# Performance work log

Measured on AMD Instinct MI355X. Metric: run time of the kernel, lower is better.

The kernel has to match this reference:

```python
import jax, jax.numpy as jnp
import numpy as np

# dims: batch, points, patches(groups), patch size, hidden, heads, layers, ffn
B, N, G, K, D, H, L, F = 32, 8192, 256, 32, 384, 6, 12, 1536
MASK_RATIO = 0.75
LEN_KEEP = int(G * (1 - MASK_RATIO))  # 64 visible tokens
HD = D // H


def _layernorm(x, g, b, eps=1e-5):
    m = jnp.mean(x, -1, keepdims=True)
    v = jnp.mean(jnp.square(x - m), -1, keepdims=True)
    return (x - m) * jax.lax.rsqrt(v + eps) * g + b


def _normalize_points(x):
    # normalize(): center = mid of bbox, radius = max distance to center (iso/diag)
    bmin = x.min(-2, keepdims=True)
    bmax = x.max(-2, keepdims=True)
    center = 0.5 * (bmin + bmax)
    radius = jnp.linalg.norm(x - center, axis=-1, keepdims=True).max(-2, keepdims=True)
    return (x - center) / radius


def _fps(x, num_samples):
    # farthest point sampling; sequential by nature -> fori_loop over G (fixed, small)
    b, n, _ = x.shape
    idxs = jnp.zeros((b, num_samples), jnp.int32)

    def body(i, state):
        dists, idxs, last = state
        lastpt = jnp.take_along_axis(x, last[:, None, None].astype(jnp.int32), axis=1)  # [B,1,3]
        d = jnp.sum(jnp.square(x - lastpt), -1)  # [B,N]
        dists = jnp.minimum(dists, d)
        nxt = jnp.argmax(dists, -1).astype(jnp.int32)
        return dists, idxs.at[:, i].set(nxt), nxt

    dists0 = jnp.full((b, n), 1e10, x.dtype)
    _, idxs, _ = jax.lax.fori_loop(1, num_samples, body, (dists0, idxs, jnp.zeros((b,), jnp.int32)))
    return idxs


def _group(x, centers):
    # squared pairwise distances without materializing [B,G,N,3]
    d2 = (jnp.sum(jnp.square(centers), -1)[:, :, None]
          + jnp.sum(jnp.square(x), -1)[:, None, :]
          - 2.0 * jnp.einsum('bgc,bnc->bgn', centers, x))  # [B,G,N]
    _, idx = jax.lax.top_k(-d2, K)  # [B,G,K] knn indices
    nbrs = jnp.take_along_axis(x[:, None, :, :], idx[..., None], axis=2)  # [B,G,K,3] (_knn_gather)
    return nbrs - centers[:, :, None, :]


def setup_inputs() -> dict:
    key = jax.random.key(0)
    ks = iter(jax.random.split(key, 24))

    def w(shape, scale=0.02):
        return jax.random.normal(next(ks), shape, jnp.float32) * scale

    ones_ln = jnp.stack([jnp.ones(D, jnp.float32), jnp.zeros(D, jnp.float32)])
    return {
        'points': jax.random.normal(next(ks), (B, N, 3), jnp.float32),
        'noise': jax.random.uniform(next(ks), (B, G), jnp.float32),
        # mini-PointNet patch encoder
        'pe_w1': w((3, 128)), 'pe_b1': jnp.zeros((128,), jnp.float32),
        'pe_w2': w((128, 256)), 'pe_b2': jnp.zeros((256,), jnp.float32),
        'pe_w3': w((256, D)), 'pe_b3': jnp.zeros((D,), jnp.float32),
        # positional MLP on patch centers
        'pos_w1': w((3, 128)), 'pos_b1': jnp.zeros((128,), jnp.float32),
        'pos_w2': w((128, D)), 'pos_b2': jnp.zeros((D,), jnp.float32),
        # transformer (stacked over L layers)
        'ln1': jnp.tile(ones_ln[None], (L, 1, 1)),
        'wqkv': w((L, D, 3 * D)), 'bqkv': jnp.zeros((L, 3 * D), jnp.float32),
        'wo': w((L, D, D)), 'bo': jnp.zeros((L, D), jnp.float32),
        'ln2': jnp.tile(ones_ln[None], (L, 1, 1)),
        'wi': w((L, D, F)), 'bi': jnp.zeros((L, F), jnp.float32),
        'wo2': w((L, F, D)), 'bo2': jnp.zeros((L, D), jnp.float32),
        'lnf': ones_ln,
    }


def _forward(points, noise, pe_w1, pe_b1, pe_w2, pe_b2, pe_w3, pe_b3,
             pos_w1, pos_b1, pos_w2, pos_b2,
             ln1, wqkv, bqkv, wo, bo, ln2, wi, bi, wo2, bo2, lnf):
    x = _normalize_points(points)
    cidx = _fps(x, G)                                        # [B,G]
    centers = jnp.take_along_axis(x, cidx[..., None], axis=1)  # [B,G,3]
    patches = _group(x, centers)                              # [B,G,K,3]

    # patch encode (per-point MLP -> max pool -> proj)
    f = jax.nn.relu(patches @ pe_w1 + pe_b1)
    f = f @ pe_w2 + pe_b2
    tokens = f.max(axis=2) @ pe_w3 + pe_b3                    # [B,G,D]
    pos = jax.nn.relu(centers @ pos_w1 + pos_b1) @ pos_w2 + pos_b2  # [B,G,D]

    # mask(): argsort-of-noise shuffle, keep first len_keep tokens
    ids_shuffle = jnp.argsort(noise, axis=1)
    ids_keep = ids_shuffle[:, :LEN_KEEP]                      # [B,64]
    h = (jnp.take_along_axis(tokens, ids_keep[..., None], axis=1)
         + jnp.take_along_axis(pos, ids_keep[..., None], axis=1))  # [B,64,D]

    scale = 1.0 / jnp.sqrt(jnp.asarray(HD, h.dtype))

    def layer(h, p):
        l1, wq, bq, wo_, bo_, l2, wi_, bi_, wo2_, bo2_ = p
        y = _layernorm(h, l1[0], l1[1])
        qkv = (y @ wq + bq).reshape(B, LEN_KEEP, 3, H, HD)  # '(three h d)' split
        q, k, v = jnp.moveaxis(qkv, 2, 0)
        a = jax.nn.softmax(jnp.einsum('bshd,bthd->bhst', q, k) * scale, -1)
        o = jnp.einsum('bhst,bthd->bshd', a, v).reshape(B, LEN_KEEP, D)
        h = h + o @ wo_ + bo_
        y = _layernorm(h, l2[0], l2[1])
        h = h + jax.nn.gelu(y @ wi_ + bi_) @ wo2_ + bo2_
        return h, None

    h, _ = jax.lax.scan(layer, h, (ln1, wqkv, bqkv, wo, bo, ln2, wi, bi, wo2, bo2))
    return _layernorm(h, lnf[0], lnf[1])


def reference(points, noise, pe_w1, pe_b1, pe_w2, pe_b2, pe_w3, pe_b3,
              pos_w1, pos_b1, pos_w2, pos_b2,
              ln1, wqkv, bqkv, wo, bo, ln2, wi, bi, wo2, bo2, lnf):
    return _forward(points, noise, pe_w1, pe_b1, pe_w2, pe_b2, pe_w3, pe_b3,
                    pos_w1, pos_b1, pos_w2, pos_b2,
                    ln1, wqkv, bqkv, wo, bo, ln2, wi, bi, wo2, bo2, lnf)
```

## Files before the change

kernel.cpp:

```cpp
#include <hip/hip_runtime.h>

#define NPTS 8192
#define NB   32
#define NG   256
#define NK   32
#define ND   384
#define NH   6
#define NLK  64
#define NF   1536
#define NHD  64
#define NL   12
#define MM   2048

typedef unsigned short u16;
typedef unsigned long long u64;
typedef __attribute__((ext_vector_type(8))) short short8;
typedef __attribute__((ext_vector_type(16))) float f32x16;
typedef __attribute__((ext_vector_type(4))) unsigned short ushort4v;

#define PL_PRE   147456ull
#define PL_LAYER 1769472ull
#define WT_ELEMS (PL_PRE + 12ull*PL_LAYER)

__device__ __forceinline__ float bf2f(u16 v){
  unsigned int u = ((unsigned int)v) << 16;
  float f; __builtin_memcpy(&f, &u, 4); return f;
}
__device__ __forceinline__ float ldf(const void* p, size_t i, bool bf){
  if(bf) return bf2f(((const u16*)p)[i]);
  return ((const float*)p)[i];
}
__device__ __forceinline__ u16 f2bf(float f){
  unsigned int x; __builtin_memcpy(&x, &f, 4);
  x += 0x7fffu + ((x >> 16) & 1u);
  return (u16)(x >> 16);
}
__device__ __forceinline__ void split2(float v, u16& hi, u16& lo){
  hi = f2bf(v);
  lo = f2bf(v - bf2f(hi));
}

__global__ __launch_bounds__(256) void k_detect(const u16* __restrict__ pts,
                                                int* __restrict__ flag){
  __shared__ int bad;
  if(threadIdx.x==0) bad=0;
  __syncthreads();
  int hit=0;
  for(int i=threadIdx.x; i<4096; i+=256){
    unsigned e = (pts[i] >> 7) & 0xFFu;
    if(e >= 0x90u) hit=1;
  }
  if(hit) atomicOr(&bad, 1);
  __syncthreads();
  if(threadIdx.x==0) *flag = bad ? 0 : 1;
}

__device__ __forceinline__ float blockMax256(float v, float* sb, int tid){
  for(int off=32; off; off>>=1) v = fmaxf(v, __shfl_down(v, off));
  __syncthreads();
  if((tid&63)==0) sb[tid>>6] = v;
  __syncthreads();
  return fmaxf(fmaxf(sb[0],sb[1]), fmaxf(sb[2],sb[3]));
}

__global__ __launch_bounds__(256) void k_normalize(const void* __restrict__ pts,
                                                   float* __restrict__ xn,
                                                   const int* __restrict__ flag){
#pragma clang fp contract(off)
  int b = blockIdx.x, tid = threadIdx.x;
  const bool bf = flag[0] != 0;
  __shared__ float sb[4];
  const size_t base = (size_t)b*NPTS*3;
  float mn0=1e30f,mn1=1e30f,mn2=1e30f, mx0=-1e30f,mx1=-1e30f,mx2=-1e30f;
  for(int n=tid; n<NPTS; n+=256){
    float x0=ldf(pts,base+n*3,bf), x1=ldf(pts,base+n*3+1,bf), x2=ldf(pts,base+n*3+2,bf);
    mn0=fminf(mn0,x0); mx0=fmaxf(mx0,x0);
    mn1=fminf(mn1,x1); mx1=fmaxf(mx1,x1);
    mn2=fminf(mn2,x2); mx2=fmaxf(mx2,x2);
  }
  mx0=blockMax256(mx0,sb,tid); mn0=-blockMax256(-mn0,sb,tid);
  mx1=blockMax256(mx1,sb,tid); mn1=-blockMax256(-mn1,sb,tid);
  mx2=blockMax256(mx2,sb,tid); mn2=-blockMax256(-mn2,sb,tid);
  float c0=0.5f*(mn0+mx0), c1=0.5f*(mn1+mx1), c2=0.5f*(mn2+mx2);
  float mr=0.0f;
  for(int n=tid; n<NPTS; n+=256){
    float d0=ldf(pts,base+n*3,bf)-c0, d1=ldf(pts,base+n*3+1,bf)-c1, d2=ldf(pts,base+n*3+2,bf)-c2;
    float nr = sqrtf((d0*d0 + d1*d1) + d2*d2);
    mr = fmaxf(mr, nr);
  }
  float radius = blockMax256(mr, sb, tid);
  float* XO = xn + base;
  for(int n=tid; n<NPTS; n+=256){
    XO[n*3  ] = (ldf(pts,base+n*3  ,bf)-c0)/radius;
    XO[n*3+1] = (ldf(pts,base+n*3+1,bf)-c1)/radius;
    XO[n*3+2] = (ldf(pts,base+n*3+2,bf)-c2)/radius;
  }
}

__global__ __launch_bounds__(256) void k_keep(const void* __restrict__ noise,
                                              int* __restrict__ keep,
                                              const int* __restrict__ flag){
  int b = blockIdx.x, g = threadIdx.x;
  const bool bf = flag[0] != 0;
  __shared__ float nv[NG];
  nv[g] = ldf(noise, (size_t)b*NG+g, bf);
  __syncthreads();
  float v = nv[g]; int r = 0;
  for(int j=0; j<NG; j++){
    float u = nv[j];
    r += (u < v) || (u == v && j < g);
  }
  if(r < NLK) keep[b*NLK + r] = g;
}

__device__ __forceinline__ void kmax_dpp_step(unsigned& hi, unsigned& lo, unsigned oh, unsigned ol){
  bool g = (oh > hi) || (oh == hi && ol > lo);
  hi = g ? oh : hi; lo = g ? ol : lo;
}
#define KMAX_DPP(CTRL) { \
  unsigned oh=(unsigned)__builtin_amdgcn_update_dpp(0,(int)kh,(CTRL),0xf,0xf,true); \
  unsigned ol=(unsigned)__builtin_amdgcn_update_dpp(0,(int)kl,(CTRL),0xf,0xf,true); \
  kmax_dpp_step(kh,kl,oh,ol); }

__global__ __launch_bounds__(512) void k_fps_trans(
    const float* __restrict__ xn, float* __restrict__ centers,
    const void* __restrict__ pe_w3, const void* __restrict__ pos_w2,
    const void* __restrict__ wqkv, const void* __restrict__ wo,
    const void* __restrict__ wi,   const void* __restrict__ wo2,
    u16* __restrict__ wthi, u16* __restrict__ wtlo,
    const int* __restrict__ flag)
{
  __shared__ float xs[NPTS*3];
  __shared__ u64 skey[3];
  __shared__ int sc[NG];
  int tid = threadIdx.x;

  if(blockIdx.x >= 32){
    const bool bf = flag[0]!=0;
    float (*t)[33] = reinterpret_cast<float(*)[33]>(xs);
    int gid = blockIdx.x - 32;
    const void* W; int Kd, Nd; size_t woff, doff; int local;
    if(gid < 96){        W=pe_w3;  Kd=256; Nd=384; woff=0; doff=0;      local=gid; }
    else if(gid < 144){  W=pos_w2; Kd=128; Nd=384; woff=0; doff=98304;  local=gid-96; }
    else{
      int g2 = gid - 144; int l = g2 / 1728; int id = g2 % 1728;
      size_t lb = PL_PRE + (size_t)l*PL_LAYER;
      if(id < 432){        W=wqkv; Kd=384;  Nd=1152; woff=(size_t)l*442368; doff=lb;          local=id; }
      else if(id < 576){   W=wo;   Kd=384;  Nd=384;  woff=(size_t)l*147456; doff=lb+442368;   local=id-432; }
      else if(id < 1152){  W=wi;   Kd=384;  Nd=1536; woff=(size_t)l*589824; doff=lb+589824;   local=id-576; }
      else {               W=wo2;  Kd=1536; Nd=384;  woff=(size_t)l*589824; doff=lb+1179648;  local=id-1152; }
    }
    int ntiles = Nd >> 5;
    int n0 = (local % ntiles)*32, k0 = (local / ntiles)*32;
    for(int i=0;i<2;i++){
      int idx = tid + i*512; int kr = idx>>5, nc = idx&31;
      t[kr][nc] = ldf(W, woff + (size_t)(k0+kr)*Nd + n0+nc, bf);
    }
    __syncthreads();
    for(int i=0;i<2;i++){
      int idx = tid + i*512; int nr = idx>>5, kc = idx&31;
      float v = t[kc][nr];
      u16 hi,lo; split2(v,hi,lo);
      size_t o = doff + (size_t)(n0+nr)*Kd + k0+kc;
      wthi[o]=hi; wtlo[o]=lo;
    }
    return;
  }

  {
#pragma clang fp contract(off)
    int b = blockIdx.x;
    int lane = tid & 63;
    const float* X = xn + (size_t)b*NPTS*3;
    float px[16],py[16],pz[16],dd[16];
#pragma unroll
    for(int s=0;s<16;s++){
      int n = s*512 + tid;
      px[s]=X[n*3]; py[s]=X[n*3+1]; pz[s]=X[n*3+2];
      dd[s]=1e10f;
    }
    for(int i=tid; i<NPTS*3; i+=512) xs[i] = X[i];
    if(tid==0){ skey[0]=0ull; skey[1]=0ull; skey[2]=0ull; sc[0]=0; }
    __syncthreads();
    float lx = xs[0], ly = xs[1], lz = xs[2];
    for(int i=1;i<NG;i++){
      int c = i % 3;
      float bv=-1.0f; int bs=0;
#pragma unroll
      for(int s=0;s<16;s++){
        float dx=px[s]-lx, dy=py[s]-ly, dz=pz[s]-lz;
        float d=(dx*dx + dy*dy) + dz*dz;
        d = fminf(dd[s], d); dd[s]=d;
        if(d > bv){ bv=d; bs=s; }
      }
      int bn = bs*512 + tid;
      unsigned kh; __builtin_memcpy(&kh,&bv,4);
      unsigned kl = (unsigned)(NPTS-1-bn);
      KMAX_DPP(0x111)
      KMAX_DPP(0x112)
      KMAX_DPP(0x114)
      KMAX_DPP(0x118)
      KMAX_DPP(0x142)
      KMAX_DPP(0x143)
      if(lane==63) atomicMax(&skey[c], ((u64)kh<<32) | (u64)kl);
      __syncthreads();
      u64 k64 = skey[c];
      int n = (NPTS-1) - (int)(k64 & 0xFFFFFFFFull);
      n &= (NPTS-1);
      if(tid==0){ sc[i]=n; skey[(i+2)%3]=0ull; }
      lx = xs[n*3]; ly = xs[n*3+1]; lz = xs[n*3+2];
    }
    __syncthreads();
    if(tid < NG){
      int n = sc[tid] & (NPTS-1);
      centers[((size_t)b*NG+tid)*3  ] = xs[n*3];
      centers[((size_t)b*NG+tid)*3+1] = xs[n*3+1];
      centers[((size_t)b*NG+tid)*3+2] = xs[n*3+2];
    }
  }
}

__global__ __launch_bounds__(256) void k_knn(
    const float* __restrict__ xn, const float* __restrict__ centers,
    const int* __restrict__ keep, float* __restrict__ patches)
{
  int blk=blockIdx.x; int b=blk>>6; int j=blk&63; int tid=threadIdx.x;
  __shared__ float sd[NPTS];
  __shared__ int   sel[NK];
  __shared__ float rv[4]; __shared__ int rn[4];
  __shared__ int   sseln;
  int g = keep[b*NLK + j] & (NG-1);
  const float* C = centers + ((size_t)b*NG + g)*3;
  float c0=C[0], c1=C[1], c2=C[2];
  const float* X = xn + (size_t)b*NPTS*3;
  {
#pragma clang fp contract(off)
    float cc = (c0*c0 + c1*c1) + c2*c2;
    for(int n=tid; n<NPTS; n+=256){
      float x0=X[n*3], x1=X[n*3+1], x2=X[n*3+2];
      float xx=(x0*x0 + x1*x1) + x2*x2;
      float dt=(c0*x0 + c1*x1) + c2*x2;
      sd[n] = (cc + xx) - 2.0f*dt;
    }
  }
  __syncthreads();
  float dl[32];
  for(int s=0;s<32;s++) dl[s] = sd[s*256 + tid];
  unsigned int alive = 0xffffffffu;
  for(int r=0; r<NK; r++){
    float bv=1e30f; int bn=0x7fffffff;
    for(int s=0;s<32;s++){
      if(alive & (1u<<s)){
        float v = dl[s];
        if(v < bv){ bv=v; bn=s*256+tid; }
      }
    }
    for(int off=32;off;off>>=1){
      float ov=__shfl_down(bv,off); int on=__shfl_down(bn,off);
      if(ov<bv || (ov==bv && on<bn)){ bv=ov; bn=on; }
    }
    if((tid&63)==0){ rv[tid>>6]=bv; rn[tid>>6]=bn; }
    __syncthreads();
    if(tid==0){
      float v=rv[0]; int n=rn[0];
      for(int w=1;w<4;w++) if(rv[w]<v || (rv[w]==v && rn[w]<n)){ v=rv[w]; n=rn[w]; }
      n &= (NPTS-1);
      sseln=n; sel[r]=n;
    }
    __syncthreads();
    int n = sseln;
    if((n & 255) == tid) alive &= ~(1u << (n >> 8));
  }
  __syncthreads();
  if(tid < NK){
    int n = sel[tid] & (NPTS-1);
    float* P = patches + ((size_t)(b*NLK+j)*NK + tid)*3;
    P[0]=X[n*3  ]-c0;
    P[1]=X[n*3+1]-c1;
    P[2]=X[n*3+2]-c2;
  }
}

__global__ __launch_bounds__(256) void k_embed(
    const float* __restrict__ patches, const float* __restrict__ centers,
    const int* __restrict__ keep,
    const void* __restrict__ w1, const void* __restrict__ b1,
    const void* __restrict__ w2, const void* __restrict__ b2,
    const void* __restrict__ pw1, const void* __restrict__ pb1,
    u16* __restrict__ mfhi, u16* __restrict__ mflo,
    u16* __restrict__ phhi, u16* __restrict__ phlo,
    const int* __restrict__ flag)
{
  int blk=blockIdx.x; int b=blk>>6; int j=blk&63; int tid=threadIdx.x;
  const bool bf = flag[0] != 0;
  __shared__ float pat[NK*3];
  __shared__ __align__(16) float f1t[128*36];
  int row = b*NLK + j;
  if(tid < NK*3) pat[tid] = patches[(size_t)row*NK*3 + tid];
  __syncthreads();
  for(int i=0;i<16;i++){
    int idx = tid + i*256;
    int k = idx>>7, m = idx&127;
    float v = ldf(b1,m,bf)
            + pat[k*3+0]*ldf(w1,        m,bf)
            + pat[k*3+1]*ldf(w1, 128 + m,bf)
            + pat[k*3+2]*ldf(w1, 256 + m,bf);
    f1t[m*36 + k] = fmaxf(v, 0.0f);
  }
  __syncthreads();
  float acc[NK];
  {
    float bv = ldf(b2, tid, bf);
#pragma unroll
    for(int k=0;k<NK;k++) acc[k]=bv;
  }
  for(int jj=0;jj<128;jj++){
    float wv = ldf(w2, (size_t)jj*256+tid, bf);
    const float* fr = &f1t[jj*36];
#pragma unroll
    for(int k8=0;k8<8;k8++){
      float4 fv = *reinterpret_cast<const float4*>(fr + k8*4);
      acc[k8*4+0] = fmaf(fv.x, wv, acc[k8*4+0]);
      acc[k8*4+1] = fmaf(fv.y, wv, acc[k8*4+1]);
      acc[k8*4+2] = fmaf(fv.z, wv, acc[k8*4+2]);
      acc[k8*4+3] = fmaf(fv.w, wv, acc[k8*4+3]);
    }
  }
  float mx = acc[0];
#pragma unroll
  for(int k=1;k<NK;k++) mx = fmaxf(mx, acc[k]);
  { u16 hi,lo; split2(mx,hi,lo);
    mfhi[(size_t)row*256 + tid]=hi; mflo[(size_t)row*256 + tid]=lo; }
  if(tid < 128){
    int g = keep[b*NLK + j] & (NG-1);
    const float* C = centers + ((size_t)b*NG + g)*3;
    float v = ldf(pb1,tid,bf)
            + C[0]*ldf(pw1,        tid,bf)
            + C[1]*ldf(pw1, 128 + tid,bf)
            + C[2]*ldf(pw1, 256 + tid,bf);
    v = fmaxf(v, 0.0f);
    u16 hi,lo; split2(v,hi,lo);
    phhi[(size_t)row*128 + tid]=hi; phlo[(size_t)row*128 + tid]=lo;
  }
}

__global__ __launch_bounds__(256) void k_transpose4(
    const void* __restrict__ wqkv, const void* __restrict__ wo,
    const void* __restrict__ wi,   const void* __restrict__ wo2,
    int l, u16* __restrict__ dhi, u16* __restrict__ dlo,
    const int* __restrict__ flag){
  __shared__ float t[32][33];
  const bool bf = flag[0]!=0;
  int id = blockIdx.x;
  const void* W; int Kd, Nd; size_t woff, doff; int local;
  if(id < 432){        W=wqkv; Kd=384;  Nd=1152; woff=(size_t)l*442368; doff=PL_PRE;          local=id; }
  else if(id < 576){   W=wo;   Kd=384;  Nd=384;  woff=(size_t)l*147456; doff=PL_PRE+442368;   local=id-432; }
  else if(id < 1152){  W=wi;   Kd=384;  Nd=1536; woff=(size_t)l*589824; doff=PL_PRE+589824;   local=id-576; }
  else {               W=wo2;  Kd=1536; Nd=384;  woff=(size_t)l*589824; doff=PL_PRE+1179648;  local=id-1152; }
  int ntiles = Nd >> 5;
  int n0 = (local % ntiles)*32, k0 = (local / ntiles)*32;
  for(int i=0;i<4;i++){
    int idx = threadIdx.x + i*256; int kr = idx>>5, nc = idx&31;
    t[kr][nc] = ldf(W, woff + (size_t)(k0+kr)*Nd + n0+nc, bf);
  }
  __syncthreads();
  for(int i=0;i<4;i++){
    int idx = threadIdx.x + i*256; int nr = idx>>5, kc = idx&31;
    float v = t[kc][nr];
    u16 hi,lo; split2(v,hi,lo);
    size_t o = doff + (size_t)(n0+nr)*Kd + k0+kc;
    dhi[o]=hi; dlo[o]=lo;
  }
}

__global__ __launch_bounds__(128) void k_ln_split(const float* __restrict__ X,
                                                  const void* __restrict__ gb, size_t go,
                                                  u16* __restrict__ Yhi, u16* __restrict__ Ylo,
                                                  const int* __restrict__ flag){
  int row=blockIdx.x, tid=threadIdx.x;
  const bool bf = flag[0] != 0;
  const float* x = X + (size_t)row*ND;
  __shared__ float sbuf[2];
  float v0=x[tid], v1=x[tid+128], v2=x[tid+256];
  float s = v0+v1+v2;
  for(int off=32;off;off>>=1) s += __shfl_down(s,off);
  if((tid&63)==0) sbuf[tid>>6]=s;
  __syncthreads();
  float mean = (sbuf[0]+sbuf[1]) * (1.0f/(float)ND);
  __syncthreads();
  float d0=v0-mean, d1=v1-mean, d2=v2-mean;
  s = d0*d0 + d1*d1 + d2*d2;
  for(int off=32;off;off>>=1) s += __shfl_down(s,off);
  if((tid&63)==0) sbuf[tid>>6]=s;
  __syncthreads();
  float var = (sbuf[0]+sbuf[1]) * (1.0f/(float)ND);
  float rstd = 1.0f / sqrtf(var + 1e-5f);
  float o0 = d0*rstd*ldf(gb,go+tid    ,bf) + ldf(gb,go+ND+tid    ,bf);
  float o1 = d1*rstd*ldf(gb,go+tid+128,bf) + ldf(gb,go+ND+tid+128,bf);
  float o2 = d2*rstd*ldf(gb,go+tid+256,bf) + ldf(gb,go+ND+tid+256,bf);
  u16 hi,lo; size_t rb = (size_t)row*ND;
  split2(o0,hi,lo); Yhi[rb+tid    ]=hi; Ylo[rb+tid    ]=lo;
  split2(o1,hi,lo); Yhi[rb+tid+128]=hi; Ylo[rb+tid+128]=lo;
  split2(o2,hi,lo); Yhi[rb+tid+256]=hi; Ylo[rb+tid+256]=lo;
}

template<int TM, int TN, int ACT, bool RES, bool OSPLIT>
__global__ __launch_bounds__(256) void k_gemm_mfma(
    const u16* __restrict__ Ahi, const u16* __restrict__ Alo,
    const u16* __restrict__ Whi, const u16* __restrict__ Wlo, size_t wo,
    const void* __restrict__ bias, size_t bo, const int* __restrict__ flag,
    const float* __restrict__ res, float* __restrict__ Cf,
    u16* __restrict__ Ohi, u16* __restrict__ Olo,
    int N, int K)
{
  __shared__ __align__(16) u16 sAh[2][64*40];
  __shared__ __align__(16) u16 sAl[2][64*40];
  __shared__ __align__(16) u16 sBh[2][64*40];
  __shared__ __align__(16) u16 sBl[2][64*40];
  int tid = threadIdx.x;
  int wave = tid >> 6, lane = tid & 63;
  int wm = wave >> 1, wn = wave & 1;
  int l31 = lane & 31, half = lane >> 5;
  int row0 = blockIdx.y*TM, col0 = blockIdx.x*TN;
  const bool bf = flag[0] != 0;
  f32x16 acc;
#pragma unroll
  for(int r=0;r<16;r++) acc[r]=0.f;

  const int sr  = tid >> 2;
  const int scc = (tid & 3) * 8;
  const u16* gAh = Ahi + (size_t)(row0+sr)*K + scc;
  const u16* gAl = Alo + (size_t)(row0+sr)*K + scc;
  const u16* gBh = Whi + wo + (size_t)(col0+sr)*K + scc;
  const u16* gBl = Wlo + wo + (size_t)(col0+sr)*K + scc;
  const int ldst = sr*40 + scc;

  uint4 rah = *reinterpret_cast<const uint4*>(gAh);
  uint4 ral = *reinterpret_cast<const uint4*>(gAl);
  uint4 rbh = *reinterpret_cast<const uint4*>(gBh);
  uint4 rbl = *reinterpret_cast<const uint4*>(gBl);

  const int nk = K >> 5;
  for(int t=0; t<nk; ++t){
    const int buf = t & 1;
    *reinterpret_cast<uint4*>(&sAh[buf][ldst]) = rah;
    *reinterpret_cast<uint4*>(&sAl[buf][ldst]) = ral;
    *reinterpret_cast<uint4*>(&sBh[buf][ldst]) = rbh;
    *reinterpret_cast<uint4*>(&sBl[buf][ldst]) = rbl;
    __syncthreads();
    if(t+1 < nk){
      const int ko = (t+1) << 5;
      rah = *reinterpret_cast<const uint4*>(gAh + ko);
      ral = *reinterpret_cast<const uint4*>(gAl + ko);
      rbh = *reinterpret_cast<const uint4*>(gBh + ko);
      rbl = *reinterpret_cast<const uint4*>(gBl + ko);
    }
#pragma unroll
    for(int ks=0; ks<2; ks++){
      int aoff = (wm*32 + l31)*40 + ks*16 + half*8;
      int boff = (wn*32 + l31)*40 + ks*16 + half*8;
      short8 ah = *reinterpret_cast<const short8*>(&sAh[buf][aoff]);
      short8 al = *reinterpret_cast<const short8*>(&sAl[buf][aoff]);
      short8 bh = *reinterpret_cast<const short8*>(&sBh[buf][boff]);
      short8 bl = *reinterpret_cast<const short8*>(&sBl[buf][boff]);
      acc = __builtin_amdgcn_mfma_f32_32x32x16_bf16(ah, bh, acc, 0,0,0);
      acc = __builtin_amdgcn_mfma_f32_32x32x16_bf16(ah, bl, acc, 0,0,0);
      acc = __builtin_amdgcn_mfma_f32_32x32x16_bf16(al, bh, acc, 0,0,0);
    }
  }
  int col = col0 + wn*32 + l31;
  float bv = ldf(bias, bo+col, bf);
#pragma unroll
  for(int r=0;r<16;r++){
    int row = row0 + wm*32 + (r&3) + 8*(r>>2) + 4*half;
    float v = acc[r] + bv;
    if(ACT==1){
      float xx = v;
      v = 0.5f*xx*(1.0f + tanhf(0.7978845608028654f*(xx + 0.044715f*xx*xx*xx)));
    }
    if(RES) v += res[(size_t)row*N + col];
    if(OSPLIT){
      u16 hi,lo; split2(v,hi,lo);
      Ohi[(size_t)row*N + col]=hi; Olo[(size_t)row*N + col]=lo;
    }else{
      Cf[(size_t)row*N + col]=v;
    }
  }
}

__global__ __launch_bounds__(256) void k_attn_pl(const float* __restrict__ qkv,
                                                 u16* __restrict__ ohi,
                                                 u16* __restrict__ olo){
  __shared__ float Qt[64*68];
  __shared__ float Kt[64*68];
  __shared__ float V [64*68];
  __shared__ float SB[64*68];
  int blk=blockIdx.x; int b=blk/NH, h=blk%NH;
  int tid=threadIdx.x;
  for(int idx=tid; idx<4096; idx+=256){
    int s=idx>>6, d=idx&63;
    const float* r = qkv + ((size_t)(b*NLK+s))*1152 + h*NHD + d;
    Qt[d*68+s]=r[0];
    Kt[d*68+s]=r[384];
    V [s*68+d]=r[768];
  }
  __syncthreads();
  {
    const int i0 = (tid>>4)*4, j0 = (tid&15)*4;
    float a00=0.f,a01=0.f,a02=0.f,a03=0.f;
    float a10=0.f,a11=0.f,a12=0.f,a13=0.f;
    float a20=0.f,a21=0.f,a22=0.f,a23=0.f;
    float a30=0.f,a31=0.f,a32=0.f,a33=0.f;
#pragma unroll 4
    for(int d=0;d<64;d++){
      float4 qa = *reinterpret_cast<const float4*>(&Qt[d*68+i0]);
      float4 kb = *reinterpret_cast<const float4*>(&Kt[d*68+j0]);
      a00=fmaf(qa.x,kb.x,a00); a01=fmaf(qa.x,kb.y,a01); a02=fmaf(qa.x,kb.z,a02); a03=fmaf(qa.x,kb.w,a03);
      a10=fmaf(qa.y,kb.x,a10); a11=fmaf(qa.y,kb.y,a11); a12=fmaf(qa.y,kb.z,a12); a13=fmaf(qa.y,kb.w,a13);
      a20=fmaf(qa.z,kb.x,a20); a21=fmaf(qa.z,kb.y,a21); a22=fmaf(qa.z,kb.z,a22); a23=fmaf(qa.z,kb.w,a23);
      a30=fmaf(qa.w,kb.x,a30); a31=fmaf(qa.w,kb.y,a31); a32=fmaf(qa.w,kb.z,a32); a33=fmaf(qa.w,kb.w,a33);
    }
    float4 o0 = {a00*0.125f, a01*0.125f, a02*0.125f, a03*0.125f};
    float4 o1 = {a10*0.125f, a11*0.125f, a12*0.125f, a13*0.125f};
    float4 o2 = {a20*0.125f, a21*0.125f, a22*0.125f, a23*0.125f};
    float4 o3 = {a30*0.125f, a31*0.125f, a32*0.125f, a33*0.125f};
    *reinterpret_cast<float4*>(&SB[(i0  )*68+j0]) = o0;
    *reinterpret_cast<float4*>(&SB[(i0+1)*68+j0]) = o1;
    *reinterpret_cast<float4*>(&SB[(i0+2)*68+j0]) = o2;
    *reinterpret_cast<float4*>(&SB[(i0+3)*68+j0]) = o3;
  }
  __syncthreads();
  if(tid<64){
    float* rowp=&SB[tid*68];
    float m=rowp[0];
    for(int j=1;j<64;j++) m=fmaxf(m,rowp[j]);
    float sum=0.0f;
    for(int j=0;j<64;j++){ float e=__expf(rowp[j]-m); rowp[j]=e; sum+=e; }
    for(int j=0;j<64;j++) Qt[j*68+tid] = rowp[j]/sum;
  }
  __syncthreads();
  {
    const int s0 = (tid>>4)*4, d0 = (tid&15)*4;
    float a00=0.f,a01=0.f,a02=0.f,a03=0.f;
    float a10=0.f,a11=0.f,a12=0.f,a13=0.f;
    float a20=0.f,a21=0.f,a22=0.f,a23=0.f;
    float a30=0.f,a31=0.f,a32=0.f,a33=0.f;
#pragma unroll 4
    for(int t=0;t<64;t++){
      float4 av = *reinterpret_cast<const float4*>(&Qt[t*68+s0]);
      float4 vv = *reinterpret_cast<const float4*>(&V [t*68+d0]);
      a00=fmaf(av.x,vv.x,a00); a01=fmaf(av.x,vv.y,a01); a02=fmaf(av.x,vv.z,a02); a03=fmaf(av.x,vv.w,a03);
      a10=fmaf(av.y,vv.x,a10); a11=fmaf(av.y,vv.y,a11); a12=fmaf(av.y,vv.z,a12); a13=fmaf(av.y,vv.w,a13);
      a20=fmaf(av.z,vv.x,a20); a21=fmaf(av.z,vv.y,a21); a22=fmaf(av.z,vv.z,a22); a23=fmaf(av.z,vv.w,a23);
      a30=fmaf(av.w,vv.x,a30); a31=fmaf(av.w,vv.y,a31); a32=fmaf(av.w,vv.z,a32); a33=fmaf(av.w,vv.w,a33);
    }
    float rr[4][4] = {{a00,a01,a02,a03},{a10,a11,a12,a13},{a20,a21,a22,a23},{a30,a31,a32,a33}};
#pragma unroll
    for(int si=0; si<4; si++){
      ushort4v h4, l4;
#pragma unroll
      for(int di=0; di<4; di++){
        u16 hi,lo; split2(rr[si][di],hi,lo);
        h4[di]=hi; l4[di]=lo;
      }
      size_t o = ((size_t)(b*NLK+s0+si))*ND + h*NHD + d0;
      *reinterpret_cast<ushort4v*>(&ohi[o]) = h4;
      *reinterpret_cast<ushort4v*>(&olo[o]) = l4;
    }
  }
}

template<bool FINAL>
__global__ __launch_bounds__(128) void k_ln(const float* __restrict__ X,
                                            const void* __restrict__ gb, size_t go,
                                            void* __restrict__ Y,
                                            const int* __restrict__ flag){
  int row=blockIdx.x, tid=threadIdx.x;
  const bool bf = flag[0] != 0;
  const float* x = X + (size_t)row*ND;
  __shared__ float sbuf[2];
  float v0=x[tid], v1=x[tid+128], v2=x[tid+256];
  float s = v0+v1+v2;
  for(int off=32;off;off>>=1) s += __shfl_down(s,off);
  if((tid&63)==0) sbuf[tid>>6]=s;
  __syncthreads();
  float mean = (sbuf[0]+sbuf[1]) * (1.0f/(float)ND);
  __syncthreads();
  float d0=v0-mean, d1=v1-mean, d2=v2-mean;
  s = d0*d0 + d1*d1 + d2*d2;
  for(int off=32;off;off>>=1) s += __shfl_down(s,off);
  if((tid&63)==0) sbuf[tid>>6]=s;
  __syncthreads();
  float var = (sbuf[0]+sbuf[1]) * (1.0f/(float)ND);
  float rstd = 1.0f / sqrtf(var + 1e-5f);
  float o0 = d0*rstd*ldf(gb,go+tid    ,bf) + ldf(gb,go+ND+tid    ,bf);
  float o1 = d1*rstd*ldf(gb,go+tid+128,bf) + ldf(gb,go+ND+tid+128,bf);
  float o2 = d2*rstd*ldf(gb,go+tid+256,bf) + ldf(gb,go+ND+tid+256,bf);
  if(FINAL && bf){
    u16* yo = (u16*)Y + (size_t)row*ND;
    yo[tid]=f2bf(o0); yo[tid+128]=f2bf(o1); yo[tid+256]=f2bf(o2);
  }else{
    float* yo = (float*)Y + (size_t)row*ND;
    yo[tid]=o0; yo[tid+128]=o1; yo[tid+256]=o2;
  }
}

extern "C" void kernel_launch(void* const* d_in, const int* in_sizes, int n_in,
                              void* d_out, int out_size, void* d_ws, size_t ws_size,
                              hipStream_t stream){
  (void)in_sizes; (void)n_in; (void)out_size;
  const void* pts   = d_in[0];
  const void* noise = d_in[1];
  const void* pe_w1 = d_in[2];
  const void* pe_b1 = d_in[3];
  const void* pe_w2 = d_in[4];
  const void* pe_b2 = d_in[5];
  const void* pe_w3 = d_in[6];
  const void* pe_b3 = d_in[7];
  const void* pos_w1= d_in[8];
  const void* pos_b1= d_in[9];
  const void* pos_w2= d_in[10];
  const void* pos_b2= d_in[11];
  const void* ln1   = d_in[12];
  const void* wqkv  = d_in[13];
  const void* bqkv  = d_in[14];
  const void* wo    = d_in[15];
  const void* bo    = d_in[16];
  const void* ln2   = d_in[17];
  const void* wi    = d_in[18];
  const void* bi    = d_in[19];
  const void* wo2   = d_in[20];
  const void* bo2   = d_in[21];
  const void* lnf   = d_in[22];

  const size_t needed_small = (6711296ull + 16) * 4;
  if (ws_size < needed_small) return;
  const size_t wt_f32_off = 6711312ull;
  const size_t needed_big = (wt_f32_off + WT_ELEMS) * 4;
  const bool big = ws_size >= needed_big;

  float* ws   = (float*)d_ws;
  float* h    = ws;
  u16*  yhi   = (u16*)(ws + 786432);
  u16*  ylo   = yhi + 786432;
  float* qkvb = ws + 1572864;
  u16*  athi  = (u16*)(ws + 3932160);
  u16*  atlo  = athi + 786432;
  u16*  ubhi  = (u16*)(ws + 1572864);
  u16*  ublo  = ubhi + 3145728;
  float* xn   = ws + 1572864;
  float* patches;
  float* centers;
  int*   keep;
  int*   flag;
  u16 *wthi, *wtlo;
  if(big){
    patches = ws + 6488064;
    centers = ws + 6684672;
    keep    = (int*)(ws + 6709248);
    flag    = (int*)(ws + 6711296);
    wthi    = (u16*)(ws + wt_f32_off);
    wtlo    = wthi + WT_ELEMS;
  }else{
    wthi    = (u16*)(ws + 4718592);
    wtlo    = (u16*)(ws + 5677056);
    patches = ws + 6635520;
    centers = ws + 6832128;
    keep    = (int*)(ws + 6856704);
    flag    = (int*)(ws + 6858752);
    if(ws_size < (6858752ull + 16) * 4) return;
  }

  k_detect   <<<1, 256, 0, stream>>>((const u16*)pts, flag);
  k_normalize<<<NB, 256, 0, stream>>>(pts, xn, flag);
  k_keep     <<<NB, 256, 0, stream>>>(noise, keep, flag);
  {
    int grid = big ? (32 + 144 + 12*1728) : (32 + 144);
    k_fps_trans<<<grid, 512, 0, stream>>>(xn, centers, pe_w3, pos_w2,
        wqkv, wo, wi, wo2, wthi, wtlo, flag);
  }
  k_knn      <<<NB*NLK, 256, 0, stream>>>(xn, centers, keep, patches);
  k_embed    <<<NB*NLK, 256, 0, stream>>>(patches, centers, keep,
      pe_w1, pe_b1, pe_w2, pe_b2, pos_w1, pos_b1,
      yhi , yhi + 2048*256 , athi , athi + 2048*128 , flag);
  k_gemm_mfma<64,64,0,false,false><<<dim3(6,32), 256, 0, stream>>>(
      yhi, yhi + 2048*256, wthi, wtlo, 0, pe_b3, 0, flag, nullptr, h, nullptr, nullptr, 384, 256);
  k_gemm_mfma<64,64,0,true ,false><<<dim3(6,32), 256, 0, stream>>>(
      athi, athi + 2048*128, wthi, wtlo, 98304, pos_b2, 0, flag, h, h, nullptr, nullptr, 384, 128);

  for(int l=0; l<NL; l++){
    size_t lb = big ? (PL_PRE + (size_t)l*PL_LAYER) : PL_PRE;
    if(!big){
      k_transpose4<<<1728, 256, 0, stream>>>(wqkv, wo, wi, wo2, l, wthi, wtlo, flag);
    }
    k_ln_split<<<MM, 128, 0, stream>>>(h, ln1, (size_t)l*2*ND, yhi, ylo, flag);
    k_gemm_mfma<64,64,0,false,false><<<dim3(18,32), 256, 0, stream>>>(
        yhi, ylo, wthi, wtlo, lb, bqkv, (size_t)l*1152, flag, nullptr, qkvb, nullptr, nullptr, 1152, 384);
    k_attn_pl<<<NB*NH, 256, 0, stream>>>(qkvb, athi, atlo);
    k_gemm_mfma<64,64,0,true ,false><<<dim3(6,32), 256, 0, stream>>>(
        athi, atlo, wthi, wtlo, lb + 442368, bo, (size_t)l*384, flag, h, h, nullptr, nullptr, 384, 384);
    k_ln_split<<<MM, 128, 0, stream>>>(h, ln2, (size_t)l*2*ND, yhi, ylo, flag);
    k_gemm_mfma<64,64,1,false,true ><<<dim3(24,32), 256, 0, stream>>>(
        yhi, ylo, wthi, wtlo, lb + 589824, bi, (size_t)l*1536, flag, nullptr, nullptr, ubhi, ublo, 1536, 384);
    k_gemm_mfma<64,64,0,true ,false><<<dim3(6,32), 256, 0, stream>>>(
        ubhi, ublo, wthi, wtlo, lb + 1179648, bo2, (size_t)l*384, flag, h, h, nullptr, nullptr, 384, 1536);
  }
  k_ln<true><<<MM, 128, 0, stream>>>(h, lnf, 0, d_out, flag);
}
```

Before: 1.815 ms.

## Shrink GEMM row tile to 32, fold keep into FPS kernel, fast GELU tanh

The MFMA GEMMs now use a 32-row tile with 128 threads. Each thread loads two B rows so the 64-column tile is still filled, and the grid doubles to give more blocks for the small M=2048 matrices. The separate k_keep launch is merged into the FPS/transpose kernel as 32 extra blocks, which removes one launch. The tanh in the GELU epilogue is replaced by an exp-based formula. This trades less A-tile reuse per block and slightly different tanh rounding for better occupancy and lower launch overhead.

```diff
diff --git a/kernel.cpp b/kernel.cpp
--- a/kernel.cpp
+++ b/kernel.cpp
@@ -97,22 +97,6 @@
   }
 }
 
-__global__ __launch_bounds__(256) void k_keep(const void* __restrict__ noise,
-                                              int* __restrict__ keep,
-                                              const int* __restrict__ flag){
-  int b = blockIdx.x, g = threadIdx.x;
-  const bool bf = flag[0] != 0;
-  __shared__ float nv[NG];
-  nv[g] = ldf(noise, (size_t)b*NG+g, bf);
-  __syncthreads();
-  float v = nv[g]; int r = 0;
-  for(int j=0; j<NG; j++){
-    float u = nv[j];
-    r += (u < v) || (u == v && j < g);
-  }
-  if(r < NLK) keep[b*NLK + r] = g;
-}
-
 __device__ __forceinline__ void kmax_dpp_step(unsigned& hi, unsigned& lo, unsigned oh, unsigned ol){
   bool g = (oh > hi) || (oh == hi && ol > lo);
   hi = g ? oh : hi; lo = g ? ol : lo;
@@ -124,6 +108,7 @@
 
 __global__ __launch_bounds__(512) void k_fps_trans(
     const float* __restrict__ xn, float* __restrict__ centers,
+    const void* __restrict__ noise, int* __restrict__ keep,
     const void* __restrict__ pe_w3, const void* __restrict__ pos_w2,
     const void* __restrict__ wqkv, const void* __restrict__ wo,
     const void* __restrict__ wi,   const void* __restrict__ wo2,
@@ -135,10 +120,10 @@
   __shared__ int sc[NG];
   int tid = threadIdx.x;
 
-  if(blockIdx.x >= 32){
+  if(blockIdx.x >= 64){
     const bool bf = flag[0]!=0;
     float (*t)[33] = reinterpret_cast<float(*)[33]>(xs);
-    int gid = blockIdx.x - 32;
+    int gid = blockIdx.x - 64;
     const void* W; int Kd, Nd; size_t woff, doff; int local;
     if(gid < 96){        W=pe_w3;  Kd=256; Nd=384; woff=0; doff=0;      local=gid; }
     else if(gid < 144){  W=pos_w2; Kd=128; Nd=384; woff=0; doff=98304;  local=gid-96; }
@@ -163,6 +148,23 @@
       u16 hi,lo; split2(v,hi,lo);
       size_t o = doff + (size_t)(n0+nr)*Kd + k0+kc;
       wthi[o]=hi; wtlo[o]=lo;
+    }
+    return;
+  }
+
+  if(blockIdx.x >= 32){
+    const bool bf = flag[0]!=0;
+    int b = blockIdx.x - 32;
+    float* nv = xs;
+    if(tid < NG) nv[tid] = ldf(noise, (size_t)b*NG+tid, bf);
+    __syncthreads();
+    if(tid < NG){
+      float v = nv[tid]; int r = 0;
+      for(int j=0; j<NG; j++){
+        float u = nv[j];
+        r += (u < v) || (u == v && j < tid);
+      }
+      if(r < NLK) keep[b*NLK + r] = tid;
     }
     return;
   }
@@ -404,8 +406,8 @@
   split2(o2,hi,lo); Yhi[rb+tid+256]=hi; Ylo[rb+tid+256]=lo;
 }
 
-template<int TM, int TN, int ACT, bool RES, bool OSPLIT>
-__global__ __launch_bounds__(256) void k_gemm_mfma(
+template<int TM, int ACT, bool RES, bool OSPLIT>
+__global__ __launch_bounds__((TM==32)?128:256) void k_gemm_mfma(
     const u16* __restrict__ Ahi, const u16* __restrict__ Alo,
     const u16* __restrict__ Whi, const u16* __restrict__ Wlo, size_t wo,
     const void* __restrict__ bias, size_t bo, const int* __restrict__ flag,
@@ -413,10 +415,11 @@
     u16* __restrict__ Ohi, u16* __restrict__ Olo,
     int N, int K)
 {
-  __shared__ __align__(16) u16 sAh[2][64*40];
-  __shared__ __align__(16) u16 sAl[2][64*40];
-  __shared__ __align__(16) u16 sBh[2][64*40];
-  __shared__ __align__(16) u16 sBl[2][64*40];
+  constexpr int TN = 64;
+  __shared__ __align__(16) u16 sAh[2][TM*40];
+  __shared__ __align__(16) u16 sAl[2][TM*40];
+  __shared__ __align__(16) u16 sBh[2][TN*40];
+  __shared__ __align__(16) u16 sBl[2][TN*40];
   int tid = threadIdx.x;
   int wave = tid >> 6, lane = tid & 63;
   int wm = wave >> 1, wn = wave & 1;
@@ -439,6 +442,11 @@
   uint4 ral = *reinterpret_cast<const uint4*>(gAl);
   uint4 rbh = *reinterpret_cast<const uint4*>(gBh);
   uint4 rbl = *reinterpret_cast<const uint4*>(gBl);
+  uint4 rbh1, rbl1;
+  if constexpr (TM==32){
+    rbh1 = *reinterpret_cast<const uint4*>(gBh + 32*(size_t)K);
+    rbl1 = *reinterpret_cast<const uint4*>(gBl + 32*(size_t)K);
+  }
 
   const int nk = K >> 5;
   for(int t=0; t<nk; ++t){
@@ -447,6 +455,10 @@
     *reinterpret_cast<uint4*>(&sAl[buf][ldst]) = ral;
     *reinterpret_cast<uint4*>(&sBh[buf][ldst]) = rbh;
     *reinterpret_cast<uint4*>(&sBl[buf][ldst]) = rbl;
+    if constexpr (TM==32){
+      *reinterpret_cast<uint4*>(&sBh[buf][ldst + 32*40]) = rbh1;
+      *reinterpret_cast<uint4*>(&sBl[buf][ldst + 32*40]) = rbl1;
+    }
     __syncthreads();
     if(t+1 < nk){
       const int ko = (t+1) << 5;
@@ -454,6 +466,10 @@
       ral = *reinterpret_cast<const uint4*>(gAl + ko);
       rbh = *reinterpret_cast<const uint4*>(gBh + ko);
       rbl = *reinterpret_cast<const uint4*>(gBl + ko);
+      if constexpr (TM==32){
+        rbh1 = *reinterpret_cast<const uint4*>(gBh + 32*(size_t)K + ko);
+        rbl1 = *reinterpret_cast<const uint4*>(gBl + 32*(size_t)K + ko);
+      }
     }
 #pragma unroll
     for(int ks=0; ks<2; ks++){
@@ -476,7 +492,12 @@
     float v = acc[r] + bv;
     if(ACT==1){
       float xx = v;
-      v = 0.5f*xx*(1.0f + tanhf(0.7978845608028654f*(xx + 0.044715f*xx*xx*xx)));
+      float u = 0.7978845608028654f*(xx + 0.044715f*xx*xx*xx);
+      float au = fabsf(u);
+      float e  = __expf(2.0f*au);
+      float th = 1.0f - 2.0f/(e + 1.0f);
+      th = (u < 0.0f) ? -th : th;
+      v = 0.5f*xx*(1.0f + th);
     }
     if(RES) v += res[(size_t)row*N + col];
     if(OSPLIT){
@@ -673,19 +694,18 @@
 
   k_detect   <<<1, 256, 0, stream>>>((const u16*)pts, flag);
   k_normalize<<<NB, 256, 0, stream>>>(pts, xn, flag);
-  k_keep     <<<NB, 256, 0, stream>>>(noise, keep, flag);
   {
-    int grid = big ? (32 + 144 + 12*1728) : (32 + 144);
-    k_fps_trans<<<grid, 512, 0, stream>>>(xn, centers, pe_w3, pos_w2,
+    int grid = big ? (64 + 144 + 12*1728) : (64 + 144);
+    k_fps_trans<<<grid, 512, 0, stream>>>(xn, centers, noise, keep, pe_w3, pos_w2,
         wqkv, wo, wi, wo2, wthi, wtlo, flag);
   }
   k_knn      <<<NB*NLK, 256, 0, stream>>>(xn, centers, keep, patches);
   k_embed    <<<NB*NLK, 256, 0, stream>>>(patches, centers, keep,
       pe_w1, pe_b1, pe_w2, pe_b2, pos_w1, pos_b1,
       yhi , yhi + 2048*256 , athi , athi + 2048*128 , flag);
-  k_gemm_mfma<64,64,0,false,false><<<dim3(6,32), 256, 0, stream>>>(
+  k_gemm_mfma<32,0,false,false><<<dim3(6,64), 128, 0, stream>>>(
       yhi, yhi + 2048*256, wthi, wtlo, 0, pe_b3, 0, flag, nullptr, h, nullptr, nullptr, 384, 256);
-  k_gemm_mfma<64,64,0,true ,false><<<dim3(6,32), 256, 0, stream>>>(
+  k_gemm_mfma<32,0,true ,false><<<dim3(6,64), 128, 0, stream>>>(
       athi, athi + 2048*128, wthi, wtlo, 98304, pos_b2, 0, flag, h, h, nullptr, nullptr, 384, 128);
 
   for(int l=0; l<NL; l++){
@@ -694,15 +714,15 @@
       k_transpose4<<<1728, 256, 0, stream>>>(wqkv, wo, wi, wo2, l, wthi, wtlo, flag);
     }
     k_ln_split<<<MM, 128, 0, stream>>>(h, ln1, (size_t)l*2*ND, yhi, ylo, flag);
-    k_gemm_mfma<64,64,0,false,false><<<dim3(18,32), 256, 0, stream>>>(
+    k_gemm_mfma<32,0,false,false><<<dim3(18,64), 128, 0, stream>>>(
         yhi, ylo, wthi, wtlo, lb, bqkv, (size_t)l*1152, flag, nullptr, qkvb, nullptr, nullptr, 1152, 384);
     k_attn_pl<<<NB*NH, 256, 0, stream>>>(qkvb, athi, atlo);
-    k_gemm_mfma<64,64,0,true ,false><<<dim3(6,32), 256, 0, stream>>>(
+    k_gemm_mfma<32,0,true ,false><<<dim3(6,64), 128, 0, stream>>>(
         athi, atlo, wthi, wtlo, lb + 442368, bo, (size_t)l*384, flag, h, h, nullptr, nullptr, 384, 384);
     k_ln_split<<<MM, 128, 0, stream>>>(h, ln2, (size_t)l*2*ND, yhi, ylo, flag);
-    k_gemm_mfma<64,64,1,false,true ><<<dim3(24,32), 256, 0, stream>>>(
+    k_gemm_mfma<32,1,false,true ><<<dim3(24,64), 128, 0, stream>>>(
         yhi, ylo, wthi, wtlo, lb + 589824, bi, (size_t)l*1536, flag, nullptr, nullptr, ubhi, ublo, 1536, 384);
-    k_gemm_mfma<64,64,0,true ,false><<<dim3(6,32), 256, 0, stream>>>(
+    k_gemm_mfma<32,0,true ,false><<<dim3(6,64), 128, 0, stream>>>(
         ubhi, ublo, wthi, wtlo, lb + 1179648, bo2, (size_t)l*384, flag, h, h, nullptr, nullptr, 384, 1536);
   }
   k_ln<true><<<MM, 128, 0, stream>>>(h, lnf, 0, d_out, flag);
```

Measured after the change: 1.888 ms. 1.04x slower.
